# Performance work log

Measured on AMD Instinct MI355X. Metric: run time of the kernel, lower is better.

The kernel has to match this reference:

```python
import jax, jax.numpy as jnp
import numpy as np

V, E, H, K = 50000, 256, 256, 16   # vocab, embed_dim, bi_lstm_hidden, n_tags (E must equal H)
HD = H // 2                        # per-direction hidden
B, NSEG, S = 32, 8, 128            # batch, segments, segment size
T = NSEG * S


def _lstm_dir(x, mask, Wih, Whh, b, h0, c0, reverse):
    """Masked (packed-equivalent) unidirectional LSTM. x:[T,B,E], mask:[T,B]."""
    def step(carry, inp):
        h, c = carry
        xt, mt = inp
        g = xt @ Wih.T + h @ Whh.T + b
        i, f, gg, o = jnp.split(g, 4, axis=-1)  # torch gate order i,f,g,o
        cn = jax.nn.sigmoid(f) * c + jax.nn.sigmoid(i) * jnp.tanh(gg)
        hn = jax.nn.sigmoid(o) * jnp.tanh(cn)
        m = mt[:, None]
        return (jnp.where(m, hn, h), jnp.where(m, cn, c)), jnp.where(m, hn, 0.0)
    (hT, cT), out = jax.lax.scan(step, (h0, c0), (x, mask), reverse=reverse)
    return out, (hT, cT)


def _bilstm(x, lengths, pf, pb, init=None):
    """pack_padded_sequence-equivalent BiLSTM. x:[T,B,E], lengths:[B]."""
    Tt, Bb = x.shape[0], x.shape[1]
    mask = jnp.arange(Tt)[:, None] < lengths[None, :]
    z = jnp.zeros((Bb, HD), x.dtype)
    h0f, c0f, h0b, c0b = init if init is not None else (z, z, z, z)
    of, (hf, cf) = _lstm_dir(x, mask, pf[0], pf[1], pf[2], h0f, c0f, False)
    ob, (hb, cb) = _lstm_dir(x, mask, pb[0], pb[1], pb[2], h0b, c0b, True)
    return jnp.concatenate([of, ob], -1), (hf, cf, hb, cb)


def _viterbi(emission, mask, start, trans, end):
    """torchcrf-style masked Viterbi decode. emission:[T,B,K], mask:[T,B]."""
    score = start[None, :] + emission[0]  # [B,K]
    def step(sc, inp):
        em, m = inp
        allsc = sc[:, :, None] + trans[None, :, :] + em[:, None, :]  # [B,K,K]
        best = jnp.max(allsc, axis=1)
        idx = jnp.argmax(allsc, axis=1).astype(jnp.int32)
        return jnp.where(m[:, None], best, sc), idx
    final, hist = jax.lax.scan(step, score, (emission[1:], mask[1:]))
    final = final + end[None, :]
    best_score = jnp.max(final, axis=-1)                 # [B]
    last = jnp.argmax(final, axis=-1).astype(jnp.int32)  # [B]
    def back(cur, inp):
        h, m = inp  # h:[B,K] backpointers at step t, m = mask[t+1]
        prev = jnp.take_along_axis(h, cur[:, None], axis=1)[:, 0]
        cur = jnp.where(m, prev, cur)
        return cur, cur
    _, tags_rev = jax.lax.scan(back, last, (hist, mask[1:]), reverse=True)
    tags = jnp.concatenate([tags_rev, last[None]], axis=0)  # [T,B]
    return tags, best_score


def _forward(texts, lengths, emb_table, Wih_f, Whh_f, bih_f, bhh_f,
             Wih_b, Whh_b, bih_b, bhh_b, Wlin, blin,
             crf_start, crf_trans, crf_end):
    pf = (Wih_f, Whh_f, bih_f + bhh_f)
    pb = (Wih_b, Whh_b, bih_b + bhh_b)
    emb = emb_table[texts]                      # [B,NSEG,S,E]
    x = jnp.transpose(emb, (1, 2, 0, 3))        # [NSEG,S,B,E]
    lens_seg = lengths.T                        # [NSEG,B]
    # pass 1: independent BiLSTM per segment (zero init state)
    outs, hids = jax.vmap(lambda xs, ls: _bilstm(xs, ls, pf, pb))(x, lens_seg)
    # positions >= per-segment max length are the raw embeddings (torch.cat with pad_text)
    maxlen = jnp.max(lens_seg, axis=1)          # [NSEG]
    over = jnp.arange(S)[None, :, None] >= maxlen[:, None, None]  # [NSEG,S,1]
    outs = jnp.where(over[..., None], x, outs)  # relies on E == 2*HD == H
    lstm1 = outs.reshape(NSEG * S, B, H)        # torch.cat(outputs, dim=0) -> [T,B,H]
    # get_text_lengths: per sample, valid tokens of all segments first, then pad tokens
    t_idx = jnp.arange(T)
    seg, pos = t_idx // S, t_idx % S
    valid = pos[None, :] < lengths[:, seg]                 # [B,T]
    key2 = jnp.where(valid, t_idx[None, :], t_idx[None, :] + T)
    perm = jnp.argsort(key2, axis=1)                       # [B,T] stable reorder
    lstm1_bt = jnp.transpose(lstm1, (1, 0, 2))             # [B,T,H]
    lstm2_in = jnp.transpose(
        jnp.take_along_axis(lstm1_bt, perm[..., None], axis=1), (1, 0, 2))  # [T,B,H]
    new_len = jnp.sum(lengths, axis=1)                     # [B]
    # pass 2: same LSTM weights, init state = final hidden of LAST segment (self.hidden)
    hf, cf, hb, cb = hids
    init = (hf[-1], cf[-1], hb[-1], cb[-1])
    lstm2_out, _ = _bilstm(lstm2_in, new_len, pf, pb, init)
    emission = lstm2_out @ Wlin.T + blin[None, None, :]    # [T,B,K]
    mask = jnp.arange(T)[:, None] < new_len[None, :]       # [T,B]
    return _viterbi(emission, mask, crf_start, crf_trans, crf_end)


def setup_inputs() -> dict:
    key = jax.random.key(0)
    ks = jax.random.split(key, 16)
    def u(k, shape, n):
        s = 1.0 / np.sqrt(n)
        return jax.random.uniform(k, shape, jnp.float32, -s, s)
    return {
        "texts": jax.random.randint(ks[0], (B, NSEG, S), 0, V).astype(jnp.int32),
        "lengths": jax.random.randint(ks[1], (B, NSEG), 1, S + 1).astype(jnp.int32),
        "emb_table": jax.random.normal(ks[2], (V, E), jnp.float32),
        "Wih_f": u(ks[3], (4 * HD, E), HD), "Whh_f": u(ks[4], (4 * HD, HD), HD),
        "bih_f": u(ks[5], (4 * HD,), HD), "bhh_f": u(ks[6], (4 * HD,), HD),
        "Wih_b": u(ks[7], (4 * HD, E), HD), "Whh_b": u(ks[8], (4 * HD, HD), HD),
        "bih_b": u(ks[9], (4 * HD,), HD), "bhh_b": u(ks[10], (4 * HD,), HD),
        "Wlin": u(ks[11], (K, H), H), "blin": u(ks[12], (K,), H),
        "crf_start": jax.random.uniform(ks[13], (K,), jnp.float32, -0.1, 0.1),
        "crf_trans": jax.random.uniform(ks[14], (K, K), jnp.float32, -0.1, 0.1),
        "crf_end": jax.random.uniform(ks[15], (K,), jnp.float32, -0.1, 0.1),
    }


def reference(texts, lengths, emb_table, Wih_f, Whh_f, bih_f, bhh_f,
              Wih_b, Whh_b, bih_b, bhh_b, Wlin, blin,
              crf_start, crf_trans, crf_end):
    # returns (tags [T,B] int32 padded with last tag beyond each length, viterbi score [B])
    return _forward(texts, lengths, emb_table, Wih_f, Whh_f, bih_f, bhh_f,
                    Wih_b, Whh_b, bih_b, bhh_b, Wlin, blin,
                    crf_start, crf_trans, crf_end)
```

## Files before the change

### kernel.cpp

```cpp
#include <hip/hip_runtime.h>
#include <cstdint>
#include <cstddef>


#define B_    32
#define NSEG_ 8
#define S_    128
#define T_    1024
#define E_    256
#define HD_   128
#define G_    512
#define K_    16
#define KS_   8

#define PIN4(v) asm volatile("" : "+v"((v).x), "+v"((v).y), "+v"((v).z), "+v"((v).w))

__global__ void prep_kernel(const int* __restrict__ lengths,
                            int* __restrict__ seg_off, int* __restrict__ new_len,
                            const float* __restrict__ bih_f, const float* __restrict__ bhh_f,
                            const float* __restrict__ bih_b, const float* __restrict__ bhh_b,
                            float* __restrict__ bias1,
                            const float* __restrict__ Wih_f, const float* __restrict__ Wih_b,
                            float* __restrict__ WT1)
{
    int gtid = blockIdx.x * blockDim.x + threadIdx.x;
    if (gtid < B_) {
        int acc = 0;
        for (int s = 0; s < NSEG_; s++) { seg_off[gtid*NSEG_ + s] = acc; acc += lengths[gtid*NSEG_ + s]; }
        new_len[gtid] = acc;
    }
    if (gtid < 1024) {
        int dir = gtid >> 9, w = gtid & 511, j = w >> 2, g = w & 3;
        int r = g * HD_ + j;
        bias1[gtid] = dir ? (bih_b[r] + bhh_b[r]) : (bih_f[r] + bhh_f[r]);
    }
    for (int e = gtid; e < 256*1024; e += gridDim.x * blockDim.x) {
        int k = e >> 10, jcol = e & 1023;
        int dir = jcol >> 9, w = jcol & 511, j = w >> 2, g = w & 3;
        int r = g * HD_ + j;
        WT1[e] = dir ? Wih_b[(size_t)r*E_ + k] : Wih_f[(size_t)r*E_ + k];
    }
}

template <int MODE>
__global__ void __launch_bounds__(256, 4)
proj_kernel(const int* __restrict__ texts, const float* __restrict__ emb,
            const float* __restrict__ WT1, const float* __restrict__ bias1,
            const float* __restrict__ lstm_packed, float* __restrict__ xproj,
            const int* __restrict__ seg_off, const int* __restrict__ new_len)
{
    int b  = blockIdx.z;
    int nl = new_len[b];
    int p0 = blockIdx.x * 32;
    if (p0 >= nl) return;
    int j0 = blockIdx.y * 256;

    __shared__ __align__(16) float As[32][256];
    __shared__ const float* rowp[32];
    int tid = threadIdx.x;
    if (tid < 32) {
        int p = p0 + tid;
        const float* r = emb;
        if (p < nl) {
            if (MODE == 0) {
                int sg = 0;
                #pragma unroll
                for (int q = 1; q < NSEG_; q++) if (seg_off[b*NSEG_ + q] <= p) sg = q;
                int t   = p - seg_off[b*NSEG_ + sg];
                int tok = texts[(b*NSEG_ + sg)*S_ + t];
                r = emb + (size_t)tok * E_;
            } else {
                r = lstm_packed + ((size_t)b*T_ + p) * 256;
            }
        }
        rowp[tid] = r;
    }
    __syncthreads();
    #pragma unroll 4
    for (int i = 0; i < 32; i++) As[i][tid] = rowp[i][tid];
    __syncthreads();

    int pg = tid >> 6;
    int jg = tid & 63;
    int j  = j0 + jg*4;
    float acc[8][4];
    #pragma unroll
    for (int i = 0; i < 8; i++) { acc[i][0]=0.f; acc[i][1]=0.f; acc[i][2]=0.f; acc[i][3]=0.f; }

    const float* wbase = WT1 + j;
    for (int k = 0; k < 256; k += 4) {
        float4 w0 = *(const float4*)(wbase + (size_t)(k+0)*1024);
        float4 w1 = *(const float4*)(wbase + (size_t)(k+1)*1024);
        float4 w2 = *(const float4*)(wbase + (size_t)(k+2)*1024);
        float4 w3 = *(const float4*)(wbase + (size_t)(k+3)*1024);
        #pragma unroll
        for (int i = 0; i < 8; i++) {
            float4 a = *(const float4*)&As[pg*8 + i][k];
            acc[i][0] = fmaf(a.w, w3.x, fmaf(a.z, w2.x, fmaf(a.y, w1.x, fmaf(a.x, w0.x, acc[i][0]))));
            acc[i][1] = fmaf(a.w, w3.y, fmaf(a.z, w2.y, fmaf(a.y, w1.y, fmaf(a.x, w0.y, acc[i][1]))));
            acc[i][2] = fmaf(a.w, w3.z, fmaf(a.z, w2.z, fmaf(a.y, w1.z, fmaf(a.x, w0.z, acc[i][2]))));
            acc[i][3] = fmaf(a.w, w3.w, fmaf(a.z, w2.w, fmaf(a.y, w1.w, fmaf(a.x, w0.w, acc[i][3]))));
        }
    }
    float4 bs = *(const float4*)(bias1 + j);
    #pragma unroll
    for (int i = 0; i < 8; i++) {
        int p = p0 + pg*8 + i;
        if (p < nl) {
            float4 r;
            r.x = acc[i][0] + bs.x; r.y = acc[i][1] + bs.y;
            r.z = acc[i][2] + bs.z; r.w = acc[i][3] + bs.w;
            *(float4*)(xproj + (((size_t)b*T_ + p) << 10) + j) = r;
        }
    }
}

__device__ __forceinline__ float sig_f(float x) { return 1.0f / (1.0f + __expf(-x)); }
__device__ __forceinline__ float tanh_f(float x) {
    float xc = fminf(fmaxf(x, -15.0f), 15.0f);
    float e  = __expf(-2.0f * xc);
    return (1.0f - e) / (1.0f + e);
}

__device__ __forceinline__ void lstm_chain(
    const float* __restrict__ Whh,
    const float* __restrict__ xp,
    float* __restrict__ outp,
    int p_base, int len, int dir, int rev,
    const float* __restrict__ h0, const float* __restrict__ c0,
    float* __restrict__ hT, float* __restrict__ cT)
{
    __shared__ __align__(16) float  h_stage[8*32];
    __shared__ __align__(16) float4 psum[2*4*HD_];

    int t = threadIdx.x;
    int w = t >> 6, L = t & 63;
    int q = w >> 1;
    int jF = t & 127;
    int r  = 32*q + (L & 31);
    bool storer = ((w & 1) == 0) && (L < 32);

    float4 wgt[4][8];
    #pragma unroll
    for (int g = 0; g < 4; g++) {
        const float4* wr = (const float4*)(Whh + (size_t)(jF + 128*g) * HD_ + 32*q);
        #pragma unroll
        for (int i = 0; i < 8; i++) { wgt[g][i] = wr[i]; PIN4(wgt[g][i]); }
    }

    float c_reg = c0 ? c0[r] : 0.0f;
    if (L < 32) h_stage[32*w + L] = h0 ? h0[32*q + L] : 0.0f;
    __syncthreads();

    const float* xb = xp + dir * G_ + 4 * r;
    float*       ob = outp + dir * HD_ + r;

    float4 xc[KS_], xn[KS_];
    float  hbuf[KS_];

    #pragma unroll
    for (int u = 0; u < KS_; u++) {
        int s = u < len ? u : (len - 1);
        int p = p_base + (rev ? (len - 1 - s) : s);
        xn[u] = *(const float4*)(xb + ((size_t)p << 10));
    }

    for (int gs = 0; gs < len; gs += KS_) {
        if (storer && gs > 0) {
            #pragma unroll
            for (int u = 0; u < KS_; u++) {
                int s = gs - KS_ + u;
                int p = p_base + (rev ? (len - 1 - s) : s);
                ob[(size_t)p * 256] = hbuf[u];
            }
        }
        #pragma unroll
        for (int u = 0; u < KS_; u++) xc[u] = xn[u];
        if (gs + KS_ < len) {
            #pragma unroll
            for (int u = 0; u < KS_; u++) {
                int s = gs + KS_ + u; s = s < len ? s : (len - 1);
                int p = p_base + (rev ? (len - 1 - s) : s);
                xn[u] = *(const float4*)(xb + ((size_t)p << 10));
            }
        }
        #pragma unroll
        for (int u = 0; u < KS_; u++) {
            int sstep = gs + u;
            if (sstep < len) {
                int par = (sstep & 1) << 9;
                const float4* hv = (const float4*)(h_stage + 32*w);
                float4 a0 = make_float4(0.f,0.f,0.f,0.f);
                float4 a1 = a0, a2 = a0, a3 = a0;
                #pragma unroll
                for (int i = 0; i < 8; i++) {
                    float4 h4 = hv[i];
                    a0.x = fmaf(h4.x, wgt[0][i].x, a0.x); a0.y = fmaf(h4.y, wgt[0][i].y, a0.y);
                    a0.z = fmaf(h4.z, wgt[0][i].z, a0.z); a0.w = fmaf(h4.w, wgt[0][i].w, a0.w);
                    a1.x = fmaf(h4.x, wgt[1][i].x, a1.x); a1.y = fmaf(h4.y, wgt[1][i].y, a1.y);
                    a1.z = fmaf(h4.z, wgt[1][i].z, a1.z); a1.w = fmaf(h4.w, wgt[1][i].w, a1.w);
                    a2.x = fmaf(h4.x, wgt[2][i].x, a2.x); a2.y = fmaf(h4.y, wgt[2][i].y, a2.y);
                    a2.z = fmaf(h4.z, wgt[2][i].z, a2.z); a2.w = fmaf(h4.w, wgt[2][i].w, a2.w);
                    a3.x = fmaf(h4.x, wgt[3][i].x, a3.x); a3.y = fmaf(h4.y, wgt[3][i].y, a3.y);
                    a3.z = fmaf(h4.z, wgt[3][i].z, a3.z); a3.w = fmaf(h4.w, wgt[3][i].w, a3.w);
                }
                psum[par + q*HD_ + jF] = make_float4((a0.x+a0.y)+(a0.z+a0.w),
                                                     (a1.x+a1.y)+(a1.z+a1.w),
                                                     (a2.x+a2.y)+(a2.z+a2.w),
                                                     (a3.x+a3.y)+(a3.z+a3.w));
                __syncthreads();
                float4 s0 = psum[par + 0*HD_ + r];
                float4 s1 = psum[par + 1*HD_ + r];
                float4 s2 = psum[par + 2*HD_ + r];
                float4 s3 = psum[par + 3*HD_ + r];
                float gi = xc[u].x + ((s0.x + s1.x) + (s2.x + s3.x));
                float gf = xc[u].y + ((s0.y + s1.y) + (s2.y + s3.y));
                float gg = xc[u].z + ((s0.z + s1.z) + (s2.z + s3.z));
                float go = xc[u].w + ((s0.w + s1.w) + (s2.w + s3.w));
                float cn = sig_f(gf) * c_reg + sig_f(gi) * tanh_f(gg);
                c_reg = cn;
                float hn = sig_f(go) * tanh_f(cn);
                if (L < 32) h_stage[32*w + L] = hn;
                hbuf[u] = hn;
                if (sstep == len - 1 && hT != nullptr && storer) {
                    hT[r] = hn; cT[r] = c_reg;
                }
            }
        }
    }
    if (storer && len > 0) {
        int gs0 = ((len - 1) / KS_) * KS_;
        #pragma unroll
        for (int u = 0; u < KS_; u++) {
            int s = gs0 + u;
            if (s < len) {
                int p = p_base + (rev ? (len - 1 - s) : s);
                ob[(size_t)p * 256] = hbuf[u];
            }
        }
    }
}

__global__ void __launch_bounds__(512, 1)
lstm1_kernel(const int* __restrict__ lengths, const int* __restrict__ seg_off,
             const float* __restrict__ Whh_f, const float* __restrict__ Whh_b,
             const float* __restrict__ xproj, float* __restrict__ lstm_packed,
             float* __restrict__ hinit, float* __restrict__ cinit)
{
    int cid = blockIdx.x;
    int b = cid >> 4, seg = (cid >> 1) & 7, dir = cid & 1;
    int len = lengths[b*NSEG_ + seg];
    int pb  = seg_off[b*NSEG_ + seg];
    const float* Whh = dir ? Whh_b : Whh_f;
    float* hT = nullptr; float* cT = nullptr;
    if (seg == NSEG_ - 1) {
        hT = hinit + (dir*B_ + b)*HD_;
        cT = cinit + (dir*B_ + b)*HD_;
    }
    lstm_chain(Whh, xproj + ((size_t)b << 20), lstm_packed + (size_t)b*T_*256,
               pb, len, dir, dir, nullptr, nullptr, hT, cT);
}

__global__ void __launch_bounds__(512, 1)
lstm2_kernel(const int* __restrict__ new_len,
             const float* __restrict__ Whh_f, const float* __restrict__ Whh_b,
             const float* __restrict__ xproj, float* __restrict__ lstm_packed,
             const float* __restrict__ hinit, const float* __restrict__ cinit)
{
    int cid = blockIdx.x;
    int b = cid >> 1, dir = cid & 1;
    int len = new_len[b];
    const float* Whh = dir ? Whh_b : Whh_f;
    lstm_chain(Whh, xproj + ((size_t)b << 20), lstm_packed + (size_t)b*T_*256,
               0, len, dir, dir,
               hinit + (dir*B_ + b)*HD_, cinit + (dir*B_ + b)*HD_,
               nullptr, nullptr);
}

__global__ void __launch_bounds__(256)
emission_kernel(const float* __restrict__ lstm_packed, const float* __restrict__ Wlin,
                const float* __restrict__ blin, float* __restrict__ emis,
                const int* __restrict__ new_len)
{
    int b  = blockIdx.y;
    int nl = new_len[b];
    int p0 = blockIdx.x * 16;
    if (p0 >= nl) return;
    int pl = threadIdx.x >> 4, s = threadIdx.x & 15;
    int p  = p0 + pl;
    const float4* xr = (const float4*)(lstm_packed + ((size_t)b*T_ + p) * 256);
    const float4* wr = (const float4*)(Wlin + (size_t)s * 256);
    float ax = 0.f, ay = 0.f, az = 0.f, aw = 0.f;
    #pragma unroll
    for (int i = 0; i < 64; i++) {
        float4 a = xr[i]; float4 ww = wr[i];
        ax = fmaf(a.x, ww.x, ax); ay = fmaf(a.y, ww.y, ay);
        az = fmaf(a.z, ww.z, az); aw = fmaf(a.w, ww.w, aw);
    }
    if (p < nl) emis[((size_t)b*T_ + p)*K_ + s] = (ax + ay) + (az + aw) + blin[s];
}

__global__ void __launch_bounds__(64)
viterbi_kernel(const float* __restrict__ emis, const float* __restrict__ start,
               const float* __restrict__ trans, const float* __restrict__ endv,
               const int* __restrict__ new_len, float* __restrict__ out)
{
    int b    = blockIdx.x;
    int nl   = new_len[b];
    int lane = threadIdx.x;
    int s    = lane & 15, q4 = lane >> 4;

    __shared__ unsigned char hist[T_ * K_];
    __shared__ unsigned char tagb[T_];

    float tr[4];
    #pragma unroll
    for (int jj = 0; jj < 4; jj++) tr[jj] = trans[(q4*4 + jj)*K_ + s];

    const float* em = emis + (size_t)b * T_ * K_;
    float sc = start[s] + em[s];

    for (int p = 1; p < nl; p++) {
        float e = em[p*K_ + s];
        float m = -3.4e38f; int a = 0;
        #pragma unroll
        for (int jj = 0; jj < 4; jj++) {
            int q   = q4*4 + jj;
            float sq = __shfl(sc, q, 16);
            float v  = sq + tr[jj];
            if (v > m) { m = v; a = q; }
        }
        #pragma unroll
        for (int d = 16; d < 64; d <<= 1) {
            float mo = __shfl_xor(m, d);
            int   ao = __shfl_xor(a, d);
            if (mo > m || (mo == m && ao < a)) { m = mo; a = ao; }
        }
        sc = m + e;
        if (lane < K_) hist[p*K_ + s] = (unsigned char)a;
    }

    float m = sc + endv[s]; int a = s;
    #pragma unroll
    for (int d = 1; d < 16; d <<= 1) {
        float mo = __shfl_xor(m, d);
        int   ao = __shfl_xor(a, d);
        if (mo > m || (mo == m && ao < a)) { m = mo; a = ao; }
    }
    int last = a;
    if (lane == 0) out[T_*B_ + b] = m;
    __syncthreads();

    for (int i = lane; i < T_; i += 64) tagb[i] = (unsigned char)last;
    __syncthreads();
    if (lane == 0) {
        int cur = last;
        for (int j = nl - 2; j >= 0; j--) {
            cur = hist[(j+1)*K_ + cur];
            tagb[j] = (unsigned char)cur;
        }
    }
    __syncthreads();
    for (int i = lane; i < T_; i += 64) out[(size_t)i*B_ + b] = (float)tagb[i];
}

extern "C" void kernel_launch(void* const* d_in, const int* in_sizes, int n_in,
                              void* d_out, int out_size, void* d_ws, size_t ws_size,
                              hipStream_t stream)
{
    (void)in_sizes; (void)n_in; (void)out_size; (void)ws_size;
    const int*   texts   = (const int*)  d_in[0];
    const int*   lengths = (const int*)  d_in[1];
    const float* emb     = (const float*)d_in[2];
    const float* Wih_f   = (const float*)d_in[3];
    const float* Whh_f   = (const float*)d_in[4];
    const float* bih_f   = (const float*)d_in[5];
    const float* bhh_f   = (const float*)d_in[6];
    const float* Wih_b   = (const float*)d_in[7];
    const float* Whh_b   = (const float*)d_in[8];
    const float* bih_b   = (const float*)d_in[9];
    const float* bhh_b   = (const float*)d_in[10];
    const float* Wlin    = (const float*)d_in[11];
    const float* blin    = (const float*)d_in[12];
    const float* c_start = (const float*)d_in[13];
    const float* c_trans = (const float*)d_in[14];
    const float* c_end   = (const float*)d_in[15];
    float* out = (float*)d_out;

    char* w = (char*)d_ws;
    int*   seg_off     = (int*)(w);
    int*   new_len     = (int*)(w + 1024);
    float* bias1       = (float*)(w + 4096);
    float* WT1         = (float*)(w + 8192);
    float* hinit       = (float*)(w + 8192 + 1048576);
    float* cinit       = hinit + 8192;
    float* lstm_packed = cinit + 8192;
    float* xproj       = lstm_packed + (size_t)B_*T_*256;
    float* emis        = xproj + ((size_t)B_ << 20);

    prep_kernel<<<128, 256, 0, stream>>>(lengths, seg_off, new_len,
                                         bih_f, bhh_f, bih_b, bhh_b, bias1,
                                         Wih_f, Wih_b, WT1);
    proj_kernel<0><<<dim3(32, 4, B_), 256, 0, stream>>>(texts, emb, WT1, bias1,
                                                        lstm_packed, xproj, seg_off, new_len);
    lstm1_kernel<<<512, 512, 0, stream>>>(lengths, seg_off, Whh_f, Whh_b,
                                          xproj, lstm_packed, hinit, cinit);
    proj_kernel<1><<<dim3(32, 4, B_), 256, 0, stream>>>(texts, emb, WT1, bias1,
                                                        lstm_packed, xproj, seg_off, new_len);
    lstm2_kernel<<<64, 512, 0, stream>>>(new_len, Whh_f, Whh_b,
                                         xproj, lstm_packed, hinit, cinit);
    emission_kernel<<<dim3(64, B_), 256, 0, stream>>>(lstm_packed, Wlin, blin, emis, new_len);
    viterbi_kernel<<<B_, 64, 0, stream>>>(emis, c_start, c_trans, c_end, new_len, out);
}
```

Baseline: 1.819 ms.

## Split LSTM recurrence across 8 K-slices with a single gate-update owner per unit

Reworks how the 512 threads of the recurrent LSTM step split the hidden-to-hidden matvec. Before, each of four quarters of the hidden dimension was handled redundantly by two waves, with double-buffered partial sums and one barrier per step. Now each wave owns a 16-wide K slice and computes two rows per lane, and only the first 128 threads reduce the 8 partials and apply the gate nonlinearity. This removes the redundant gate computation and the psum double buffer, but adds a second barrier per step and an 8-way reduction on half the threads. The x-prefetch depth is also reduced from 8 to 4 steps.

```diff
diff --git a/kernel.cpp b/kernel.cpp
--- a/kernel.cpp
+++ b/kernel.cpp
@@ -11,7 +11,7 @@
 #define HD_   128
 #define G_    512
 #define K_    16
-#define KS_   8
+#define KS_   4
 
 #define PIN4(v) asm volatile("" : "+v"((v).x), "+v"((v).y), "+v"((v).z), "+v"((v).w))
 
@@ -130,105 +130,128 @@
     const float* __restrict__ h0, const float* __restrict__ c0,
     float* __restrict__ hT, float* __restrict__ cT)
 {
-    __shared__ __align__(16) float  h_stage[8*32];
-    __shared__ __align__(16) float4 psum[2*4*HD_];
+    __shared__ __align__(16) float  h_sh[HD_];
+    __shared__ __align__(16) float4 psum[8*HD_];
 
     int t = threadIdx.x;
     int w = t >> 6, L = t & 63;
-    int q = w >> 1;
-    int jF = t & 127;
-    int r  = 32*q + (L & 31);
-    bool storer = ((w & 1) == 0) && (L < 32);
-
-    float4 wgt[4][8];
-    #pragma unroll
-    for (int g = 0; g < 4; g++) {
-        const float4* wr = (const float4*)(Whh + (size_t)(jF + 128*g) * HD_ + 32*q);
-        #pragma unroll
-        for (int i = 0; i < 8; i++) { wgt[g][i] = wr[i]; PIN4(wgt[g][i]); }
-    }
-
-    float c_reg = c0 ? c0[r] : 0.0f;
-    if (L < 32) h_stage[32*w + L] = h0 ? h0[32*q + L] : 0.0f;
-    __syncthreads();
-
-    const float* xb = xp + dir * G_ + 4 * r;
-    float*       ob = outp + dir * HD_ + r;
+    int ks = 16 * w;
+
+    float4 wgt[2][4][4];
+    #pragma unroll
+    for (int rr = 0; rr < 2; rr++) {
+        int row = L + 64*rr;
+        #pragma unroll
+        for (int g = 0; g < 4; g++) {
+            const float4* wp = (const float4*)(Whh + (size_t)(g*HD_ + row)*HD_ + ks);
+            #pragma unroll
+            for (int i = 0; i < 4; i++) { wgt[rr][g][i] = wp[i]; PIN4(wgt[rr][g][i]); }
+        }
+    }
+
+    float c_reg = 0.0f;
+    if (t < HD_) {
+        h_sh[t] = h0 ? h0[t] : 0.0f;
+        c_reg   = c0 ? c0[t] : 0.0f;
+    }
+    __syncthreads();
+
+    const float* xb = xp + dir * G_ + 4 * t;
+    float*       ob = outp + dir * HD_ + t;
 
     float4 xc[KS_], xn[KS_];
     float  hbuf[KS_];
 
-    #pragma unroll
-    for (int u = 0; u < KS_; u++) {
-        int s = u < len ? u : (len - 1);
-        int p = p_base + (rev ? (len - 1 - s) : s);
-        xn[u] = *(const float4*)(xb + ((size_t)p << 10));
+    if (t < HD_) {
+        #pragma unroll
+        for (int u = 0; u < KS_; u++) {
+            int s = u < len ? u : (len - 1);
+            int p = p_base + (rev ? (len - 1 - s) : s);
+            xn[u] = *(const float4*)(xb + ((size_t)p << 10));
+        }
     }
 
     for (int gs = 0; gs < len; gs += KS_) {
-        if (storer && gs > 0) {
+        if (t < HD_) {
+            if (gs > 0) {
+                #pragma unroll
+                for (int u = 0; u < KS_; u++) {
+                    int s = gs - KS_ + u;
+                    int p = p_base + (rev ? (len - 1 - s) : s);
+                    ob[(size_t)p * 256] = hbuf[u];
+                }
+            }
             #pragma unroll
-            for (int u = 0; u < KS_; u++) {
-                int s = gs - KS_ + u;
-                int p = p_base + (rev ? (len - 1 - s) : s);
-                ob[(size_t)p * 256] = hbuf[u];
-            }
-        }
-        #pragma unroll
-        for (int u = 0; u < KS_; u++) xc[u] = xn[u];
-        if (gs + KS_ < len) {
-            #pragma unroll
-            for (int u = 0; u < KS_; u++) {
-                int s = gs + KS_ + u; s = s < len ? s : (len - 1);
-                int p = p_base + (rev ? (len - 1 - s) : s);
-                xn[u] = *(const float4*)(xb + ((size_t)p << 10));
+            for (int u = 0; u < KS_; u++) xc[u] = xn[u];
+            if (gs + KS_ < len) {
+                #pragma unroll
+                for (int u = 0; u < KS_; u++) {
+                    int s = gs + KS_ + u; s = s < len ? s : (len - 1);
+                    int p = p_base + (rev ? (len - 1 - s) : s);
+                    xn[u] = *(const float4*)(xb + ((size_t)p << 10));
+                }
             }
         }
         #pragma unroll
         for (int u = 0; u < KS_; u++) {
             int sstep = gs + u;
             if (sstep < len) {
-                int par = (sstep & 1) << 9;
-                const float4* hv = (const float4*)(h_stage + 32*w);
-                float4 a0 = make_float4(0.f,0.f,0.f,0.f);
-                float4 a1 = a0, a2 = a0, a3 = a0;
+                const float4* hv = (const float4*)(h_sh + ks);
+                float4 q0 = make_float4(0.f,0.f,0.f,0.f);
+                float4 q1 = q0, q2 = q0, q3 = q0;
+                float4 Q0 = q0, Q1 = q0, Q2 = q0, Q3 = q0;
                 #pragma unroll
-                for (int i = 0; i < 8; i++) {
+                for (int i = 0; i < 4; i++) {
                     float4 h4 = hv[i];
-                    a0.x = fmaf(h4.x, wgt[0][i].x, a0.x); a0.y = fmaf(h4.y, wgt[0][i].y, a0.y);
-                    a0.z = fmaf(h4.z, wgt[0][i].z, a0.z); a0.w = fmaf(h4.w, wgt[0][i].w, a0.w);
-                    a1.x = fmaf(h4.x, wgt[1][i].x, a1.x); a1.y = fmaf(h4.y, wgt[1][i].y, a1.y);
-                    a1.z = fmaf(h4.z, wgt[1][i].z, a1.z); a1.w = fmaf(h4.w, wgt[1][i].w, a1.w);
-                    a2.x = fmaf(h4.x, wgt[2][i].x, a2.x); a2.y = fmaf(h4.y, wgt[2][i].y, a2.y);
-                    a2.z = fmaf(h4.z, wgt[2][i].z, a2.z); a2.w = fmaf(h4.w, wgt[2][i].w, a2.w);
-                    a3.x = fmaf(h4.x, wgt[3][i].x, a3.x); a3.y = fmaf(h4.y, wgt[3][i].y, a3.y);
-                    a3.z = fmaf(h4.z, wgt[3][i].z, a3.z); a3.w = fmaf(h4.w, wgt[3][i].w, a3.w);
+                    q0.x=fmaf(h4.x,wgt[0][0][i].x,q0.x); q0.y=fmaf(h4.y,wgt[0][0][i].y,q0.y);
+                    q0.z=fmaf(h4.z,wgt[0][0][i].z,q0.z); q0.w=fmaf(h4.w,wgt[0][0][i].w,q0.w);
+                    q1.x=fmaf(h4.x,wgt[0][1][i].x,q1.x); q1.y=fmaf(h4.y,wgt[0][1][i].y,q1.y);
+                    q1.z=fmaf(h4.z,wgt[0][1][i].z,q1.z); q1.w=fmaf(h4.w,wgt[0][1][i].w,q1.w);
+                    q2.x=fmaf(h4.x,wgt[0][2][i].x,q2.x); q2.y=fmaf(h4.y,wgt[0][2][i].y,q2.y);
+                    q2.z=fmaf(h4.z,wgt[0][2][i].z,q2.z); q2.w=fmaf(h4.w,wgt[0][2][i].w,q2.w);
+                    q3.x=fmaf(h4.x,wgt[0][3][i].x,q3.x); q3.y=fmaf(h4.y,wgt[0][3][i].y,q3.y);
+                    q3.z=fmaf(h4.z,wgt[0][3][i].z,q3.z); q3.w=fmaf(h4.w,wgt[0][3][i].w,q3.w);
+                    Q0.x=fmaf(h4.x,wgt[1][0][i].x,Q0.x); Q0.y=fmaf(h4.y,wgt[1][0][i].y,Q0.y);
+                    Q0.z=fmaf(h4.z,wgt[1][0][i].z,Q0.z); Q0.w=fmaf(h4.w,wgt[1][0][i].w,Q0.w);
+                    Q1.x=fmaf(h4.x,wgt[1][1][i].x,Q1.x); Q1.y=fmaf(h4.y,wgt[1][1][i].y,Q1.y);
+                    Q1.z=fmaf(h4.z,wgt[1][1][i].z,Q1.z); Q1.w=fmaf(h4.w,wgt[1][1][i].w,Q1.w);
+                    Q2.x=fmaf(h4.x,wgt[1][2][i].x,Q2.x); Q2.y=fmaf(h4.y,wgt[1][2][i].y,Q2.y);
+                    Q2.z=fmaf(h4.z,wgt[1][2][i].z,Q2.z); Q2.w=fmaf(h4.w,wgt[1][2][i].w,Q2.w);
+                    Q3.x=fmaf(h4.x,wgt[1][3][i].x,Q3.x); Q3.y=fmaf(h4.y,wgt[1][3][i].y,Q3.y);
+                    Q3.z=fmaf(h4.z,wgt[1][3][i].z,Q3.z); Q3.w=fmaf(h4.w,wgt[1][3][i].w,Q3.w);
                 }
-                psum[par + q*HD_ + jF] = make_float4((a0.x+a0.y)+(a0.z+a0.w),
-                                                     (a1.x+a1.y)+(a1.z+a1.w),
-                                                     (a2.x+a2.y)+(a2.z+a2.w),
-                                                     (a3.x+a3.y)+(a3.z+a3.w));
+                psum[w*HD_ + L] = make_float4((q0.x+q0.y)+(q0.z+q0.w),
+                                              (q1.x+q1.y)+(q1.z+q1.w),
+                                              (q2.x+q2.y)+(q2.z+q2.w),
+                                              (q3.x+q3.y)+(q3.z+q3.w));
+                psum[w*HD_ + L + 64] = make_float4((Q0.x+Q0.y)+(Q0.z+Q0.w),
+                                                   (Q1.x+Q1.y)+(Q1.z+Q1.w),
+                                                   (Q2.x+Q2.y)+(Q2.z+Q2.w),
+                                                   (Q3.x+Q3.y)+(Q3.z+Q3.w));
                 __syncthreads();
-                float4 s0 = psum[par + 0*HD_ + r];
-                float4 s1 = psum[par + 1*HD_ + r];
-                float4 s2 = psum[par + 2*HD_ + r];
-                float4 s3 = psum[par + 3*HD_ + r];
-                float gi = xc[u].x + ((s0.x + s1.x) + (s2.x + s3.x));
-                float gf = xc[u].y + ((s0.y + s1.y) + (s2.y + s3.y));
-                float gg = xc[u].z + ((s0.z + s1.z) + (s2.z + s3.z));
-                float go = xc[u].w + ((s0.w + s1.w) + (s2.w + s3.w));
-                float cn = sig_f(gf) * c_reg + sig_f(gi) * tanh_f(gg);
-                c_reg = cn;
-                float hn = sig_f(go) * tanh_f(cn);
-                if (L < 32) h_stage[32*w + L] = hn;
-                hbuf[u] = hn;
-                if (sstep == len - 1 && hT != nullptr && storer) {
-                    hT[r] = hn; cT[r] = c_reg;
+                if (t < HD_) {
+                    float4 sa = psum[t];
+                    #pragma unroll
+                    for (int sl = 1; sl < 8; sl++) {
+                        float4 p4 = psum[sl*HD_ + t];
+                        sa.x += p4.x; sa.y += p4.y; sa.z += p4.z; sa.w += p4.w;
+                    }
+                    float gi = xc[u].x + sa.x;
+                    float gf = xc[u].y + sa.y;
+                    float gg = xc[u].z + sa.z;
+                    float go = xc[u].w + sa.w;
+                    float cn = sig_f(gf) * c_reg + sig_f(gi) * tanh_f(gg);
+                    c_reg = cn;
+                    float hn = sig_f(go) * tanh_f(cn);
+                    h_sh[t] = hn;
+                    hbuf[u] = hn;
+                    if (sstep == len - 1 && hT != nullptr) { hT[t] = hn; cT[t] = c_reg; }
                 }
+                __syncthreads();
             }
         }
     }
-    if (storer && len > 0) {
+    if (t < HD_ && len > 0) {
         int gs0 = ((len - 1) / KS_) * KS_;
         #pragma unroll
         for (int u = 0; u < KS_; u++) {
```

Measured after the change: 1.747 ms. 4.0% less time.

## Restructure LSTM recurrence to wave-local shuffle reduction with double-buffered hidden state

Applied to the files above, without the earlier changes.

Reassigns work in the recurrent LSTM chain so that each wave owns 16 hidden units, with 4 lane groups splitting the K dimension. Partial gate sums are now reduced with cross-lane shuffles instead of a shared-memory psum buffer, and the gate math is split across lane pairs. The hidden state is double-buffered in LDS, so each step needs one barrier after the h write rather than a barrier plus the psum round-trip. A rotated weight/h index is intended to avoid LDS bank conflicts. Sigmoid and tanh now use hardware reciprocal with one Newton step, which slightly changes numerics.

```diff
diff --git a/kernel.cpp b/kernel.cpp
--- a/kernel.cpp
+++ b/kernel.cpp
@@ -14,6 +14,13 @@
 #define KS_   8
 
 #define PIN4(v) asm volatile("" : "+v"((v).x), "+v"((v).y), "+v"((v).z), "+v"((v).w))
+
+__device__ __forceinline__ float fast_rcp(float x) {
+    float r;
+    asm("v_rcp_f32 %0, %1" : "=v"(r) : "v"(x));
+    r = r * (2.0f - x * r);
+    return r;
+}
 
 __global__ void prep_kernel(const int* __restrict__ lengths,
                             int* __restrict__ seg_off, int* __restrict__ new_len,
@@ -115,13 +122,6 @@
     }
 }
 
-__device__ __forceinline__ float sig_f(float x) { return 1.0f / (1.0f + __expf(-x)); }
-__device__ __forceinline__ float tanh_f(float x) {
-    float xc = fminf(fmaxf(x, -15.0f), 15.0f);
-    float e  = __expf(-2.0f * xc);
-    return (1.0f - e) / (1.0f + e);
-}
-
 __device__ __forceinline__ void lstm_chain(
     const float* __restrict__ Whh,
     const float* __restrict__ xp,
@@ -130,43 +130,44 @@
     const float* __restrict__ h0, const float* __restrict__ c0,
     float* __restrict__ hT, float* __restrict__ cT)
 {
-    __shared__ __align__(16) float  h_stage[8*32];
-    __shared__ __align__(16) float4 psum[2*4*HD_];
-
-    int t = threadIdx.x;
-    int w = t >> 6, L = t & 63;
-    int q = w >> 1;
-    int jF = t & 127;
-    int r  = 32*q + (L & 31);
-    bool storer = ((w & 1) == 0) && (L < 32);
+    __shared__ __align__(16) float h_sh[2*HD_];
+
+    int t  = threadIdx.x;
+    int w  = t >> 6, L = t & 63;
+    int kq = L >> 4;
+    int rl = L & 15;
+    int r  = 16*w + rl;
+    int odd = kq & 1;
+    int rot = 2 * kq;
 
     float4 wgt[4][8];
     #pragma unroll
     for (int g = 0; g < 4; g++) {
-        const float4* wr = (const float4*)(Whh + (size_t)(jF + 128*g) * HD_ + 32*q);
-        #pragma unroll
-        for (int i = 0; i < 8; i++) { wgt[g][i] = wr[i]; PIN4(wgt[g][i]); }
-    }
-
-    float c_reg = c0 ? c0[r] : 0.0f;
-    if (L < 32) h_stage[32*w + L] = h0 ? h0[32*q + L] : 0.0f;
-    __syncthreads();
-
-    const float* xb = xp + dir * G_ + 4 * r;
+        const float4* wp = (const float4*)(Whh + (size_t)(g*HD_ + r)*HD_ + 32*kq);
+        #pragma unroll
+        for (int i = 0; i < 8; i++) { wgt[g][i] = wp[(rot + i) & 7]; PIN4(wgt[g][i]); }
+    }
+
+    float c_reg = 0.0f;
+    if (!odd) c_reg = c0 ? c0[r] : 0.0f;
+    if (L < 16) h_sh[r] = h0 ? h0[r] : 0.0f;
+    __syncthreads();
+
+    const float* xb = xp + dir * G_ + 4*r + 2*odd;
     float*       ob = outp + dir * HD_ + r;
 
-    float4 xc[KS_], xn[KS_];
+    float2 xc[KS_], xn[KS_];
     float  hbuf[KS_];
 
     #pragma unroll
     for (int u = 0; u < KS_; u++) {
         int s = u < len ? u : (len - 1);
         int p = p_base + (rev ? (len - 1 - s) : s);
-        xn[u] = *(const float4*)(xb + ((size_t)p << 10));
+        xn[u] = *(const float2*)(xb + ((size_t)p << 10));
     }
 
     for (int gs = 0; gs < len; gs += KS_) {
-        if (storer && gs > 0) {
+        if (L < 16 && gs > 0) {
             #pragma unroll
             for (int u = 0; u < KS_; u++) {
                 int s = gs - KS_ + u;
@@ -181,54 +182,64 @@
             for (int u = 0; u < KS_; u++) {
                 int s = gs + KS_ + u; s = s < len ? s : (len - 1);
                 int p = p_base + (rev ? (len - 1 - s) : s);
-                xn[u] = *(const float4*)(xb + ((size_t)p << 10));
+                xn[u] = *(const float2*)(xb + ((size_t)p << 10));
             }
         }
         #pragma unroll
         for (int u = 0; u < KS_; u++) {
             int sstep = gs + u;
             if (sstep < len) {
-                int par = (sstep & 1) << 9;
-                const float4* hv = (const float4*)(h_stage + 32*w);
+                int par = (sstep & 1) * HD_;
+                const float* hb = h_sh + par + 32*kq;
                 float4 a0 = make_float4(0.f,0.f,0.f,0.f);
                 float4 a1 = a0, a2 = a0, a3 = a0;
                 #pragma unroll
                 for (int i = 0; i < 8; i++) {
-                    float4 h4 = hv[i];
-                    a0.x = fmaf(h4.x, wgt[0][i].x, a0.x); a0.y = fmaf(h4.y, wgt[0][i].y, a0.y);
-                    a0.z = fmaf(h4.z, wgt[0][i].z, a0.z); a0.w = fmaf(h4.w, wgt[0][i].w, a0.w);
-                    a1.x = fmaf(h4.x, wgt[1][i].x, a1.x); a1.y = fmaf(h4.y, wgt[1][i].y, a1.y);
-                    a1.z = fmaf(h4.z, wgt[1][i].z, a1.z); a1.w = fmaf(h4.w, wgt[1][i].w, a1.w);
-                    a2.x = fmaf(h4.x, wgt[2][i].x, a2.x); a2.y = fmaf(h4.y, wgt[2][i].y, a2.y);
-                    a2.z = fmaf(h4.z, wgt[2][i].z, a2.z); a2.w = fmaf(h4.w, wgt[2][i].w, a2.w);
-                    a3.x = fmaf(h4.x, wgt[3][i].x, a3.x); a3.y = fmaf(h4.y, wgt[3][i].y, a3.y);
-                    a3.z = fmaf(h4.z, wgt[3][i].z, a3.z); a3.w = fmaf(h4.w, wgt[3][i].w, a3.w);
+                    float4 h4 = *(const float4*)(hb + 4*((rot + i) & 7));
+                    a0.x=fmaf(h4.x,wgt[0][i].x,a0.x); a0.y=fmaf(h4.y,wgt[0][i].y,a0.y);
+                    a0.z=fmaf(h4.z,wgt[0][i].z,a0.z); a0.w=fmaf(h4.w,wgt[0][i].w,a0.w);
+                    a1.x=fmaf(h4.x,wgt[1][i].x,a1.x); a1.y=fmaf(h4.y,wgt[1][i].y,a1.y);
+                    a1.z=fmaf(h4.z,wgt[1][i].z,a1.z); a1.w=fmaf(h4.w,wgt[1][i].w,a1.w);
+                    a2.x=fmaf(h4.x,wgt[2][i].x,a2.x); a2.y=fmaf(h4.y,wgt[2][i].y,a2.y);
+                    a2.z=fmaf(h4.z,wgt[2][i].z,a2.z); a2.w=fmaf(h4.w,wgt[2][i].w,a2.w);
+                    a3.x=fmaf(h4.x,wgt[3][i].x,a3.x); a3.y=fmaf(h4.y,wgt[3][i].y,a3.y);
+                    a3.z=fmaf(h4.z,wgt[3][i].z,a3.z); a3.w=fmaf(h4.w,wgt[3][i].w,a3.w);
                 }
-                psum[par + q*HD_ + jF] = make_float4((a0.x+a0.y)+(a0.z+a0.w),
-                                                     (a1.x+a1.y)+(a1.z+a1.w),
-                                                     (a2.x+a2.y)+(a2.z+a2.w),
-                                                     (a3.x+a3.y)+(a3.z+a3.w));
-                __syncthreads();
-                float4 s0 = psum[par + 0*HD_ + r];
-                float4 s1 = psum[par + 1*HD_ + r];
-                float4 s2 = psum[par + 2*HD_ + r];
-                float4 s3 = psum[par + 3*HD_ + r];
-                float gi = xc[u].x + ((s0.x + s1.x) + (s2.x + s3.x));
-                float gf = xc[u].y + ((s0.y + s1.y) + (s2.y + s3.y));
-                float gg = xc[u].z + ((s0.z + s1.z) + (s2.z + s3.z));
-                float go = xc[u].w + ((s0.w + s1.w) + (s2.w + s3.w));
-                float cn = sig_f(gf) * c_reg + sig_f(gi) * tanh_f(gg);
+                float p0 = (a0.x+a0.y)+(a0.z+a0.w);
+                float p1 = (a1.x+a1.y)+(a1.z+a1.w);
+                float p2 = (a2.x+a2.y)+(a2.z+a2.w);
+                float p3 = (a3.x+a3.y)+(a3.z+a3.w);
+                float sx = __shfl_xor(odd ? p0 : p2, 16);
+                float sy = __shfl_xor(odd ? p1 : p3, 16);
+                float qa = (odd ? p2 : p0) + sx;
+                float qb = (odd ? p3 : p1) + sy;
+                qa += __shfl_xor(qa, 32);
+                qb += __shfl_xor(qb, 32);
+                qa += xc[u].x;
+                qb += xc[u].y;
+                float qc  = fminf(fmaxf(qa, -15.0f), 15.0f);
+                float e1  = __expf(odd ? -2.0f*qc : -qa);
+                float num = odd ? (1.0f - e1) : 1.0f;
+                float ah  = num * fast_rcp(1.0f + e1);
+                float bh  = fast_rcp(1.0f + __expf(-qb));
+                float gh  = __shfl_xor(ah, 16);
+                float oh  = __shfl_xor(bh, 16);
+                float cn  = bh * c_reg + ah * gh;
                 c_reg = cn;
-                float hn = sig_f(go) * tanh_f(cn);
-                if (L < 32) h_stage[32*w + L] = hn;
+                float cc  = fminf(fmaxf(cn, -15.0f), 15.0f);
+                float e3  = __expf(-2.0f * cc);
+                float th  = (1.0f - e3) * fast_rcp(1.0f + e3);
+                float hn  = oh * th;
+                if (L < 16) h_sh[(par ^ HD_) + r] = hn;
                 hbuf[u] = hn;
-                if (sstep == len - 1 && hT != nullptr && storer) {
+                if (sstep == len - 1 && hT != nullptr && L < 16) {
                     hT[r] = hn; cT[r] = c_reg;
                 }
+                __syncthreads();
             }
         }
     }
-    if (storer && len > 0) {
+    if (L < 16 && len > 0) {
         int gs0 = ((len - 1) / KS_) * KS_;
         #pragma unroll
         for (int u = 0; u < KS_; u++) {
```

Result: faster. 1.658 ms (-8.8%).
